# Kernel optimization log

Measured on AMD Instinct MI355X. Metric: run time of the kernel, lower is better.

## Reference

```python
import jax, jax.numpy as jnp
import numpy as np

N_NODES = 16384
N_EDGES = 262144
N_GRAPHS = 64
COLORS = 16
EMB = 256
HEADS = 8
FFN = 1024
LAYERS = 4
LMAX = 320


def _ln(x, g, b, eps=1e-5):
    m = x.mean(-1, keepdims=True)
    v = x.var(-1, keepdims=True)
    return (x - m) * jax.lax.rsqrt(v + eps) * g + b


def setup_inputs() -> dict:
    key = jax.random.key(0)
    ks = iter(jax.random.split(key, 64))
    s = 0.05
    def rn(shape):
        return jax.random.normal(next(ks), shape, jnp.float32) * s
    # 64 graphs: 32 with 192 nodes, 32 with 320 nodes -> total 16384, L_max=320
    lengths = np.concatenate([np.full(32, 192, np.int64), np.full(32, 320, np.int64)])
    batches = jnp.asarray(np.concatenate([[0], np.cumsum(lengths)]).astype(np.int32))
    x = jax.random.normal(next(ks), (N_NODES, COLORS), jnp.float32)
    edge_index = jax.random.randint(next(ks), (2, N_EDGES), 0, N_NODES, jnp.int32)
    inp = dict(
        x=x, edge_index=edge_index, batches=batches, L_max=LMAX,
        sW0=rn((COLORS, EMB)), sWn0=rn((COLORS, EMB)), sb0=jnp.zeros(EMB),
        sW1=rn((EMB, EMB)), sWn1=rn((EMB, EMB)), sb1=jnp.zeros(EMB),
        sW2=rn((EMB, EMB)), sWn2=rn((EMB, EMB)), sb2=jnp.zeros(EMB),
        Wq=rn((LAYERS, EMB, EMB)), Wk=rn((LAYERS, EMB, EMB)), Wv=rn((LAYERS, EMB, EMB)),
        bq=jnp.zeros((LAYERS, EMB)), bk=jnp.zeros((LAYERS, EMB)), bv=jnp.zeros((LAYERS, EMB)),
        Wo=rn((LAYERS, EMB, EMB)), bo=jnp.zeros((LAYERS, EMB)),
        ln1g=jnp.ones((LAYERS, EMB)), ln1b=jnp.zeros((LAYERS, EMB)),
        ln2g=jnp.ones((LAYERS, EMB)), ln2b=jnp.zeros((LAYERS, EMB)),
        W1=rn((LAYERS, EMB, FFN)), b1=jnp.zeros((LAYERS, FFN)),
        W2=rn((LAYERS, FFN, EMB)), b2=jnp.zeros((LAYERS, EMB)),
    )
    return inp


def reference(x, edge_index, batches, L_max,
              sW0, sWn0, sb0, sW1, sWn1, sb1, sW2, sWn2, sb2,
              Wq, Wk, Wv, bq, bk, bv, Wo, bo,
              ln1g, ln1b, ln2g, ln2b, W1, b1, W2, b2):
    N = x.shape[0]
    src, dst = edge_index[0], edge_index[1]
    deg = jnp.maximum(
        jax.ops.segment_sum(jnp.ones(src.shape[0], x.dtype), dst, num_segments=N), 1.0
    )[:, None]

    def sage(h, Ws, Wn, b, act):
        agg = jax.ops.segment_sum(h[src], dst, num_segments=N) / deg  # mean neighbor agg
        h2 = h @ Ws + agg @ Wn + b
        return jax.nn.relu(h2) if act else h2

    z = sage(x, sW0, sWn0, sb0, True)
    z = sage(z, sW1, sWn1, sb1, True)
    z = sage(z, sW2, sWn2, sb2, False)

    # pack_and_pad (intended semantics): seq-first [L_max, n_graphs, D] + key padding mask
    nG = batches.shape[0] - 1
    lengths = batches[1:] - batches[:-1]
    ids = jnp.arange(N)
    seg = jnp.searchsorted(batches, ids, side='right') - 1  # graph id per node
    pos = ids - batches[seg]                                 # position within graph
    D = z.shape[1]
    h = jnp.zeros((L_max, nG, D), z.dtype).at[pos, seg].set(z)
    pad = jnp.arange(L_max)[None, :] >= lengths[:, None]     # [nG, L_max], True = padded

    H = HEADS
    dh = D // H
    scale = 1.0 / np.sqrt(dh).astype(np.float32)
    for l in range(Wq.shape[0]):
        L, Bg = h.shape[0], h.shape[1]
        q = (h @ Wq[l] + bq[l]).reshape(L, Bg, H, dh)
        k = (h @ Wk[l] + bk[l]).reshape(L, Bg, H, dh)
        v = (h @ Wv[l] + bv[l]).reshape(L, Bg, H, dh)
        sc = jnp.einsum('lbhd,mbhd->bhlm', q, k) * scale
        sc = jnp.where(pad[:, None, None, :], -1e9, sc)
        a = jax.nn.softmax(sc, axis=-1)
        o = jnp.einsum('bhlm,mbhd->lbhd', a, v).reshape(L, Bg, D) @ Wo[l] + bo[l]
        h = _ln(h + o, ln1g[l], ln1b[l])
        ff = jax.nn.relu(h @ W1[l] + b1[l]) @ W2[l] + b2[l]
        h = _ln(h + ff, ln2g[l], ln2b[l])
    return h
```

## Files before the change

### kernel.cpp

```cpp
#include <hip/hip_runtime.h>
#include <hip/hip_bf16.h>
#include <math.h>

#define NN  16384
#define NE  262144
#define NG  64
#define CIN 16
#define DD  256
#define NHD 8
#define DHD 32
#define DFF 1024
#define NLY 4
#define LM  320
#define QS  768
#define QKW 512
#define NV  16384
#define NRV 16512

typedef __attribute__((ext_vector_type(8))) short bf16x8;
typedef __attribute__((ext_vector_type(4))) float f32x4;

__device__ __forceinline__ unsigned short f2bf(float f) {
    union { __hip_bfloat16 h; unsigned short u; } cv;
    cv.h = __float2bfloat16(f);
    return cv.u;
}
__device__ __forceinline__ float bf2f(unsigned short u) {
    return __uint_as_float((unsigned int)u << 16);
}
__device__ __forceinline__ void gl_lds16(const unsigned short* g, unsigned short* l) {
    __builtin_amdgcn_global_load_lds(
        (const __attribute__((address_space(1))) unsigned int*)g,
        (__attribute__((address_space(3))) unsigned int*)l, 16, 0, 0);
}
__device__ __forceinline__ int gsearch(const int* __restrict__ batches, int row) {
    int lo = 0, hi = NG;
    while (lo < hi) {
        int mid = (lo + hi + 1) >> 1;
        if (batches[mid] <= row) lo = mid; else hi = mid - 1;
    }
    return lo;
}

__global__ void zero_ws_kernel(uint4* __restrict__ hbp, uint4* __restrict__ obp,
                               int* __restrict__ counts) {
    int i = blockIdx.x * 256 + threadIdx.x;
    if (i < 4096) {
        hbp[i] = (uint4){0u, 0u, 0u, 0u};
        obp[i] = (uint4){0u, 0u, 0u, 0u};
    }
    if (i < NN) counts[i] = 0;
}

__global__ __launch_bounds__(256) void prep_all_kernel(
    const float* __restrict__ Wq, const float* __restrict__ Wk, const float* __restrict__ Wv,
    const float* __restrict__ Wo, const float* __restrict__ W1, const float* __restrict__ W2,
    const float* __restrict__ sW1, const float* __restrict__ sWn1,
    const float* __restrict__ sW2, const float* __restrict__ sWn2,
    const float* __restrict__ bq, const float* __restrict__ bk, const float* __restrict__ bv,
    unsigned short* __restrict__ Wqkvt, unsigned short* __restrict__ Wot,
    unsigned short* __restrict__ W1t, unsigned short* __restrict__ W2t,
    unsigned short* __restrict__ sW1t, unsigned short* __restrict__ sWn1t,
    unsigned short* __restrict__ sW2t, unsigned short* __restrict__ sWn2t,
    float* __restrict__ bqkvp)
{
    const int t = threadIdx.x;
    int bid = blockIdx.x;
    if (bid < 12) {
        int i = bid * 256 + t;
        if (i < NLY * QS) {
            int n = i % QS, l = i / QS;
            const float* b = (n < 256) ? bq : (n < 512 ? bk : bv);
            float v = b[l * DD + (n & 255)];
            if (n < 256) v *= 0.17677669529663687f;
            bqkvp[i] = v;
        }
        return;
    }
    bid -= 12;
    __shared__ float Ls[64][68];
    const float* inP;
    unsigned short* outP;
    int strideIn, strideOut;
    float sc = 1.f;
    if (bid < 192) {
        int x = bid % 12, y = (bid / 12) % 4, l = bid / 48;
        int n0 = x * 64, k0 = y * 64;
        const float* W = (n0 < 256) ? Wq : (n0 < 512 ? Wk : Wv);
        if (n0 < 256) sc = 0.17677669529663687f;
        inP  = W + ((size_t)l * DD + k0) * DD + (n0 & 255);
        strideIn = DD;
        outP = Wqkvt + ((size_t)l * QS + n0) * DD + k0;
        strideOut = DD;
    } else if (bid < 192 + 64) {
        bid -= 192;
        int x = bid % 4, y = (bid / 4) % 4, l = bid / 16;
        int n0 = x * 64, k0 = y * 64;
        inP  = Wo + ((size_t)l * DD + k0) * DD + n0;
        strideIn = DD;
        outP = Wot + ((size_t)l * DD + n0) * DD + k0;
        strideOut = DD;
    } else if (bid < 192 + 64 + 256) {
        bid -= 192 + 64;
        int x = bid % 16, y = (bid / 16) % 4, l = bid / 64;
        int n0 = x * 64, k0 = y * 64;
        inP  = W1 + ((size_t)l * DD + k0) * DFF + n0;
        strideIn = DFF;
        outP = W1t + ((size_t)l * DFF + n0) * DD + k0;
        strideOut = DD;
    } else if (bid < 192 + 64 + 512) {
        bid -= 192 + 64 + 256;
        int x = bid % 4, y = (bid / 4) % 16, l = bid / 64;
        int n0 = x * 64, k0 = y * 64;
        inP  = W2 + ((size_t)l * DFF + k0) * DD + n0;
        strideIn = DD;
        outP = W2t + ((size_t)l * DD + n0) * DFF + k0;
        strideOut = DFF;
    } else {
        bid -= 192 + 64 + 512;
        int w = bid / 16, r = bid % 16;
        int x = r % 4, y = r / 4;
        int n0 = x * 64, k0 = y * 64;
        const float* src = (w == 0) ? sW1 : (w == 1) ? sWn1 : (w == 2) ? sW2 : sWn2;
        unsigned short* dst = (w == 0) ? sW1t : (w == 1) ? sWn1t : (w == 2) ? sW2t : sWn2t;
        inP  = src + (size_t)k0 * DD + n0;
        strideIn = DD;
        outP = dst + (size_t)n0 * DD + k0;
        strideOut = DD;
    }
    #pragma unroll
    for (int it = 0; it < 4; ++it) {
        int lin = it * 256 + t;
        int kr = lin >> 4, nc = (lin & 15) * 4;
        float4 v = *(const float4*)&inP[(size_t)kr * strideIn + nc];
        Ls[kr][nc]     = v.x * sc;
        Ls[kr][nc + 1] = v.y * sc;
        Ls[kr][nc + 2] = v.z * sc;
        Ls[kr][nc + 3] = v.w * sc;
    }
    __syncthreads();
    #pragma unroll
    for (int it = 0; it < 2; ++it) {
        int lin = it * 256 + t;
        int nr = lin >> 3, kc = (lin & 7) * 8;
        unsigned short pk[8];
        #pragma unroll
        for (int j = 0; j < 8; ++j) pk[j] = f2bf(Ls[kc + j][nr]);
        *(uint4*)&outP[(size_t)nr * strideOut + kc] = *(uint4*)pk;
    }
}

__global__ void count_edges_kernel(const int* __restrict__ dst, int* __restrict__ counts) {
    int e = blockIdx.x * 256 + threadIdx.x;
    if (e < NE) atomicAdd(&counts[dst[e]], 1);
}

__global__ __launch_bounds__(1024) void scan_kernel(const int* __restrict__ counts,
                                                    int* __restrict__ offsets,
                                                    int* __restrict__ cursor) {
    __shared__ int part[1024];
    int t = threadIdx.x;
    int base = t * 16;
    int s = 0;
    #pragma unroll
    for (int i = 0; i < 16; ++i) s += counts[base + i];
    part[t] = s;
    __syncthreads();
    for (int off = 1; off < 1024; off <<= 1) {
        int val = (t >= off) ? part[t - off] : 0;
        __syncthreads();
        part[t] += val;
        __syncthreads();
    }
    int run = (t == 0) ? 0 : part[t - 1];
    #pragma unroll
    for (int i = 0; i < 16; ++i) {
        offsets[base + i] = run;
        cursor[base + i]  = run;
        run += counts[base + i];
    }
    if (t == 1023) offsets[NN] = run;
}

__global__ void fill_csr_kernel(const int* __restrict__ src, const int* __restrict__ dst,
                                int* __restrict__ cursor, int* __restrict__ csr) {
    int e = blockIdx.x * 256 + threadIdx.x;
    if (e < NE) {
        int p = atomicAdd(&cursor[dst[e]], 1);
        csr[p] = src[e];
    }
}

__global__ __launch_bounds__(256) void agg_mean16_kernel(
    const float* __restrict__ h, const int* __restrict__ offsets,
    const int* __restrict__ csr, float* __restrict__ out)
{
    int node = blockIdx.x * 16 + (threadIdx.x >> 4);
    int d = threadIdx.x & 15;
    int beg = offsets[node], end = offsets[node + 1];
    float acc = 0.f;
    int e = beg;
    for (; e + 1 < end; e += 2) {
        float v0 = h[(size_t)csr[e] * CIN + d];
        float v1 = h[(size_t)csr[e + 1] * CIN + d];
        acc += v0 + v1;
    }
    if (e < end) acc += h[(size_t)csr[e] * CIN + d];
    int dg = end - beg; if (dg < 1) dg = 1;
    out[(size_t)node * CIN + d] = acc * (1.f / (float)dg);
}

__global__ __launch_bounds__(256) void agg_mean_b_kernel(
    const unsigned short* __restrict__ h, const int* __restrict__ offsets,
    const int* __restrict__ csr, unsigned short* __restrict__ out)
{
    int node = blockIdx.x * 4 + (threadIdx.x >> 6);
    int lane = threadIdx.x & 63;
    int half = lane >> 5;
    int hl   = lane & 31;
    int beg = offsets[node], end = offsets[node + 1];
    float a[8] = {0.f, 0.f, 0.f, 0.f, 0.f, 0.f, 0.f, 0.f};
    int e = beg + half;
    for (; e + 2 < end; e += 4) {
        bf16x8 h0 = *(const bf16x8*)(h + (size_t)csr[e] * DD + hl * 8);
        bf16x8 h1 = *(const bf16x8*)(h + (size_t)csr[e + 2] * DD + hl * 8);
        #pragma unroll
        for (int j = 0; j < 8; ++j) a[j] += bf2f((unsigned short)h0[j]);
        #pragma unroll
        for (int j = 0; j < 8; ++j) a[j] += bf2f((unsigned short)h1[j]);
    }
    if (e < end) {
        bf16x8 h0 = *(const bf16x8*)(h + (size_t)csr[e] * DD + hl * 8);
        #pragma unroll
        for (int j = 0; j < 8; ++j) a[j] += bf2f((unsigned short)h0[j]);
    }
    #pragma unroll
    for (int j = 0; j < 8; ++j) a[j] += __shfl_xor(a[j], 32, 64);
    int dg = end - beg; if (dg < 1) dg = 1;
    float inv = 1.f / (float)dg;
    if (half == 0) {
        unsigned short pk[8];
        #pragma unroll
        for (int j = 0; j < 8; ++j) pk[j] = f2bf(a[j] * inv);
        *(uint4*)(out + (size_t)node * DD + hl * 8) = *(uint4*)pk;
    }
}

template <int ACT, bool DUAL>
__global__ __launch_bounds__(256) void gemm_f32b_kernel(
    const float* __restrict__ A, const float* __restrict__ W,
    const float* __restrict__ A2, const float* __restrict__ W2,
    const float* __restrict__ bias, unsigned short* __restrict__ Cb,
    int M, int N, int K)
{
    __shared__ __align__(16) float As[16][64];
    __shared__ __align__(16) float Ws[16][64];
    const int t  = threadIdx.x;
    const int tx = t & 15, ty = t >> 4;
    const int m0 = blockIdx.y * 64, n0 = blockIdx.x * 64;
    const int arow = t >> 2, acol = (t & 3) * 4;
    const int wrow = t >> 4, wcol = (t & 15) * 4;
    float acc[4][4] = {};
    const int npass = DUAL ? 2 : 1;
    for (int pass = 0; pass < npass; ++pass) {
        const float* Ap = (DUAL && pass) ? A2 : A;
        const float* Wp = (DUAL && pass) ? W2 : W;
        for (int k0 = 0; k0 < K; k0 += 16) {
            __syncthreads();
            float4 av = *(const float4*)(Ap + (size_t)(m0 + arow) * K + k0 + acol);
            As[acol + 0][arow] = av.x;
            As[acol + 1][arow] = av.y;
            As[acol + 2][arow] = av.z;
            As[acol + 3][arow] = av.w;
            *(float4*)&Ws[wrow][wcol] = *(const float4*)(Wp + (size_t)(k0 + wrow) * N + n0 + wcol);
            __syncthreads();
            #pragma unroll
            for (int kk = 0; kk < 16; ++kk) {
                float4 a4 = *(const float4*)&As[kk][ty * 4];
                float4 b4 = *(const float4*)&Ws[kk][tx * 4];
                float aa[4] = {a4.x, a4.y, a4.z, a4.w};
                float bb[4] = {b4.x, b4.y, b4.z, b4.w};
                #pragma unroll
                for (int i = 0; i < 4; ++i)
                    #pragma unroll
                    for (int j = 0; j < 4; ++j)
                        acc[i][j] += aa[i] * bb[j];
            }
        }
    }
    float4 bv = *(const float4*)(bias + n0 + tx * 4);
    float bb4[4] = {bv.x, bv.y, bv.z, bv.w};
    #pragma unroll
    for (int i = 0; i < 4; ++i) {
        float c[4];
        #pragma unroll
        for (int j = 0; j < 4; ++j) {
            c[j] = acc[i][j] + bb4[j];
            if (ACT == 1) c[j] = fmaxf(c[j], 0.f);
        }
        ushort4 ov;
        ov.x = f2bf(c[0]); ov.y = f2bf(c[1]); ov.z = f2bf(c[2]); ov.w = f2bf(c[3]);
        *(ushort4*)(Cb + (size_t)(m0 + ty * 4 + i) * N + n0 + tx * 4) = ov;
    }
}

template <int ACT, bool DUAL>
__global__ __launch_bounds__(256) void mfma_gemm_kernel(
    const unsigned short* __restrict__ A,  const unsigned short* __restrict__ Wt,
    const unsigned short* __restrict__ A2, const unsigned short* __restrict__ Wt2,
    const float* __restrict__ bias, unsigned short* __restrict__ Cb,
    int M, int N, int K)
{
    __shared__ __align__(16) unsigned short As[128 * 64];
    __shared__ __align__(16) unsigned short Bs[128 * 64];
    const int t = threadIdx.x;
    const int wave = t >> 6, lane = t & 63;
    const int quad = lane >> 4, r16 = lane & 15;
    const int wr = (wave >> 1) * 64, wc = (wave & 1) * 64;
    const int m0 = blockIdx.y * 128, n0 = blockIdx.x * 128;
    const int srow = t >> 3;
    const int scol = ((t & 7) * 8) ^ ((srow & 7) << 3);
    const int swz  = (r16 & 7) << 3;

    f32x4 acc[4][4];
    #pragma unroll
    for (int i = 0; i < 4; ++i)
        #pragma unroll
        for (int j = 0; j < 4; ++j)
            acc[i][j] = (f32x4){0.f, 0.f, 0.f, 0.f};

    const int npass = DUAL ? 2 : 1;
    for (int pass = 0; pass < npass; ++pass) {
        const unsigned short* Ap = (DUAL && pass) ? A2 : A;
        const unsigned short* Wp = (DUAL && pass) ? Wt2 : Wt;
        for (int k0 = 0; k0 < K; k0 += 64) {
            __syncthreads();
            #pragma unroll
            for (int c = 0; c < 4; ++c) {
                gl_lds16(&Ap[(size_t)(m0 + c * 32 + srow) * K + k0 + scol],
                         As + c * 2048 + wave * 512);
                gl_lds16(&Wp[(size_t)(n0 + c * 32 + srow) * K + k0 + scol],
                         Bs + c * 2048 + wave * 512);
            }
            __syncthreads();
            #pragma unroll
            for (int kk = 0; kk < 2; ++kk) {
                const int cofs = (kk * 32 + quad * 8) ^ swz;
                bf16x8 af[4], bfr[4];
                #pragma unroll
                for (int i = 0; i < 4; ++i)
                    af[i] = *(const bf16x8*)&As[(wr + i * 16 + r16) * 64 + cofs];
                #pragma unroll
                for (int j = 0; j < 4; ++j)
                    bfr[j] = *(const bf16x8*)&Bs[(wc + j * 16 + r16) * 64 + cofs];
                #pragma unroll
                for (int i = 0; i < 4; ++i)
                    #pragma unroll
                    for (int j = 0; j < 4; ++j)
                        acc[i][j] = __builtin_amdgcn_mfma_f32_16x16x32_bf16(
                            af[i], bfr[j], acc[i][j], 0, 0, 0);
            }
        }
    }

    float bcol[4];
    #pragma unroll
    for (int j = 0; j < 4; ++j) bcol[j] = bias[n0 + wc + j * 16 + r16];
    #pragma unroll
    for (int i = 0; i < 4; ++i) {
        const int rowb = m0 + wr + i * 16 + quad * 4;
        #pragma unroll
        for (int rr = 0; rr < 4; ++rr) {
            const size_t rb = (size_t)(rowb + rr) * N;
            #pragma unroll
            for (int j = 0; j < 4; ++j) {
                float v = acc[i][j][rr] + bcol[j];
                if (ACT == 1) v = fmaxf(v, 0.f);
                Cb[rb + n0 + wc + j * 16 + r16] = f2bf(v);
            }
        }
    }
}

__global__ __launch_bounds__(256) void gemm_qkv_kernel(
    const unsigned short* __restrict__ A, const unsigned short* __restrict__ Wt,
    const float* __restrict__ bias, const int* __restrict__ batches,
    unsigned short* __restrict__ QKb, unsigned short* __restrict__ Vt, int K)
{
    __shared__ __align__(16) unsigned short As[128 * 64];
    __shared__ __align__(16) unsigned short Bs[128 * 64];
    const int t = threadIdx.x;
    const int wave = t >> 6, lane = t & 63;
    const int quad = lane >> 4, r16 = lane & 15;
    const int wr = (wave >> 1) * 64, wc = (wave & 1) * 64;
    const int m0 = blockIdx.y * 128, n0 = blockIdx.x * 128;
    const int srow = t >> 3;
    const int scol = ((t & 7) * 8) ^ ((srow & 7) << 3);
    const int swz  = (r16 & 7) << 3;

    f32x4 acc[4][4];
    #pragma unroll
    for (int i = 0; i < 4; ++i)
        #pragma unroll
        for (int j = 0; j < 4; ++j)
            acc[i][j] = (f32x4){0.f, 0.f, 0.f, 0.f};

    for (int k0 = 0; k0 < K; k0 += 64) {
        __syncthreads();
        #pragma unroll
        for (int c = 0; c < 4; ++c) {
            gl_lds16(&A[(size_t)(m0 + c * 32 + srow) * K + k0 + scol],
                     As + c * 2048 + wave * 512);
            gl_lds16(&Wt[(size_t)(n0 + c * 32 + srow) * K + k0 + scol],
                     Bs + c * 2048 + wave * 512);
        }
        __syncthreads();
        #pragma unroll
        for (int kk = 0; kk < 2; ++kk) {
            const int cofs = (kk * 32 + quad * 8) ^ swz;
            bf16x8 af[4], bfr[4];
            #pragma unroll
            for (int i = 0; i < 4; ++i)
                af[i] = *(const bf16x8*)&As[(wr + i * 16 + r16) * 64 + cofs];
            #pragma unroll
            for (int j = 0; j < 4; ++j)
                bfr[j] = *(const bf16x8*)&Bs[(wc + j * 16 + r16) * 64 + cofs];
            #pragma unroll
            for (int i = 0; i < 4; ++i)
                #pragma unroll
                for (int j = 0; j < 4; ++j)
                    acc[i][j] = __builtin_amdgcn_mfma_f32_16x16x32_bf16(
                        af[i], bfr[j], acc[i][j], 0, 0, 0);
        }
    }

    float bcol[4];
    #pragma unroll
    for (int j = 0; j < 4; ++j) bcol[j] = bias[n0 + wc + j * 16 + r16];

    if (n0 < 512) {
        #pragma unroll
        for (int i = 0; i < 4; ++i) {
            const int rowb = m0 + wr + i * 16 + quad * 4;
            #pragma unroll
            for (int rr = 0; rr < 4; ++rr) {
                const size_t rb = (size_t)(rowb + rr) * QKW;
                #pragma unroll
                for (int j = 0; j < 4; ++j)
                    QKb[rb + n0 + wc + j * 16 + r16] = f2bf(acc[i][j][rr] + bcol[j]);
            }
        }
    } else {
        #pragma unroll
        for (int i = 0; i < 4; ++i) {
            const int rowb = m0 + wr + i * 16 + quad * 4;
            if (rowb >= NV) continue;
            const int g = gsearch(batches, rowb);
            const int key = rowb - batches[g];
            #pragma unroll
            for (int j = 0; j < 4; ++j) {
                const int dim = n0 - 512 + wc + j * 16 + r16;
                unsigned short pk[4];
                #pragma unroll
                for (int rr = 0; rr < 4; ++rr) pk[rr] = f2bf(acc[i][j][rr] + bcol[j]);
                *(uint2*)&Vt[((size_t)g * DD + dim) * LM + key] = *(uint2*)pk;
            }
        }
    }
}

template <bool PERM>
__global__ __launch_bounds__(512) void gemm_ln_kernel(
    const unsigned short* __restrict__ A, const unsigned short* __restrict__ Wt,
    const float* __restrict__ bias, const unsigned short* __restrict__ residb,
    const float* __restrict__ gam, const float* __restrict__ bet,
    const int* __restrict__ batches,
    float* __restrict__ outF, float* __restrict__ repO,
    unsigned short* __restrict__ outHb, int K)
{
    __shared__ __align__(16) unsigned short As[64 * 64];
    __shared__ __align__(16) unsigned short Bs[256 * 64];
    __shared__ float red[2][4][64];
    const int t = threadIdx.x;
    const int wave = t >> 6, lane = t & 63;
    const int quad = lane >> 4, r16 = lane & 15;
    const int wr = (wave >> 2) * 32;
    const int wc = (wave & 3) * 64;
    const int m0 = blockIdx.x * 64;
    const int srow = t >> 3;
    const int scol = ((t & 7) * 8) ^ ((srow & 7) << 3);
    const int swz  = (r16 & 7) << 3;

    f32x4 acc[2][4];
    #pragma unroll
    for (int i = 0; i < 2; ++i)
        #pragma unroll
        for (int j = 0; j < 4; ++j)
            acc[i][j] = (f32x4){0.f, 0.f, 0.f, 0.f};

    for (int k0 = 0; k0 < K; k0 += 64) {
        __syncthreads();
        gl_lds16(&A[(size_t)(m0 + srow) * K + k0 + scol], As + wave * 512);
        #pragma unroll
        for (int c = 0; c < 4; ++c)
            gl_lds16(&Wt[(size_t)(c * 64 + srow) * K + k0 + scol],
                     Bs + c * 4096 + wave * 512);
        __syncthreads();
        #pragma unroll
        for (int kk = 0; kk < 2; ++kk) {
            const int cofs = (kk * 32 + quad * 8) ^ swz;
            bf16x8 af[2], bfr[4];
            #pragma unroll
            for (int i = 0; i < 2; ++i)
                af[i] = *(const bf16x8*)&As[(wr + i * 16 + r16) * 64 + cofs];
            #pragma unroll
            for (int j = 0; j < 4; ++j)
                bfr[j] = *(const bf16x8*)&Bs[(wc + j * 16 + r16) * 64 + cofs];
            #pragma unroll
            for (int i = 0; i < 2; ++i)
                #pragma unroll
                for (int j = 0; j < 4; ++j)
                    acc[i][j] = __builtin_amdgcn_mfma_f32_16x16x32_bf16(
                        af[i], bfr[j], acc[i][j], 0, 0, 0);
        }
    }

    float bcol[4];
    #pragma unroll
    for (int j = 0; j < 4; ++j) bcol[j] = bias[wc + j * 16 + r16];

    #pragma unroll
    for (int i = 0; i < 2; ++i) {
        const int row = wr + i * 16 + quad * 4;
        #pragma unroll
        for (int rr = 0; rr < 4; ++rr) {
            const size_t rb = (size_t)(m0 + row + rr) * DD;
            float s1 = 0.f, s2 = 0.f;
            #pragma unroll
            for (int j = 0; j < 4; ++j) {
                float v = acc[i][j][rr] + bcol[j] + bf2f(residb[rb + wc + j * 16 + r16]);
                acc[i][j][rr] = v;
                s1 += v;
                s2 += v * v;
            }
            #pragma unroll
            for (int off = 1; off < 16; off <<= 1) {
                s1 += __shfl_xor(s1, off, 64);
                s2 += __shfl_xor(s2, off, 64);
            }
            if (r16 == 0) {
                red[0][wave & 3][row + rr] = s1;
                red[1][wave & 3][row + rr] = s2;
            }
        }
    }
    __syncthreads();

    int gg = 0, posb = 0;
    if (PERM && m0 < NV) {
        gg = gsearch(batches, m0);
        posb = m0 - batches[gg];
    }
    #pragma unroll
    for (int i = 0; i < 2; ++i) {
        const int row = wr + i * 16 + quad * 4;
        #pragma unroll
        for (int rr = 0; rr < 4; ++rr) {
            const int lr = row + rr;
            const int gr = m0 + lr;
            float s1 = red[0][0][lr] + red[0][1][lr] + red[0][2][lr] + red[0][3][lr];
            float s2 = red[1][0][lr] + red[1][1][lr] + red[1][2][lr] + red[1][3][lr];
            float mean = s1 * (1.f / 256.f);
            float var  = s2 * (1.f / 256.f) - mean * mean;
            float rs = rsqrtf(var + 1e-5f);
            const size_t hb = (size_t)gr * DD;
            #pragma unroll
            for (int j = 0; j < 4; ++j) {
                const int col = wc + j * 16 + r16;
                float ov = (acc[i][j][rr] - mean) * rs * gam[col] + bet[col];
                if (PERM) {
                    if (m0 < NV) {
                        outF[((size_t)(posb + lr) * NG + gg) * DD + col] = ov;
                    } else {
                        int g2 = m0 - NV + lr;
                        if (g2 < NG) repO[(size_t)g2 * DD + col] = ov;
                    }
                } else {
                    outHb[hb + col] = f2bf(ov);
                }
            }
        }
    }
}

__global__ __launch_bounds__(256) void attn_mfma_kernel(
    const unsigned short* __restrict__ qk, const unsigned short* __restrict__ vt,
    const int* __restrict__ batches, unsigned short* __restrict__ o)
{
    __shared__ __align__(16) unsigned short Pa[4][64 * 40];
    const int bx = blockIdx.x;
    const int tile = bx >> 1;
    const int row0 = tile * 64;
    const int tid = threadIdx.x;
    const int wave = tid >> 6;
    const int h = (bx & 1) * 4 + wave;
    const int lane = tid & 63;
    const int quad = lane >> 4, r16 = lane & 15;
    const int g = gsearch(batches, row0);
    const int len = batches[g + 1] - batches[g];
    const size_t gq = (size_t)batches[g];
    unsigned short* pa = Pa[wave];

    bf16x8 qf[4];
    #pragma unroll
    for (int i = 0; i < 4; ++i)
        qf[i] = *(const bf16x8*)(qk + (size_t)(row0 + i * 16 + r16) * QKW + h * 32 + quad * 8);
    bf16x8 onesf;
    #pragma unroll
    for (int j = 0; j < 8; ++j) onesf[j] = (short)0x3F80;

    f32x4 oacc[4][2], lacc[4];
    #pragma unroll
    for (int i = 0; i < 4; ++i) {
        lacc[i] = (f32x4){0.f, 0.f, 0.f, 0.f};
        #pragma unroll
        for (int nt = 0; nt < 2; ++nt)
            oacc[i][nt] = (f32x4){0.f, 0.f, 0.f, 0.f};
    }

    for (int t0 = 0; t0 < len; t0 += 32) {
        bf16x8 kf[2], vf[2];
        #pragma unroll
        for (int mt = 0; mt < 2; ++mt)
            kf[mt] = *(const bf16x8*)(qk + (gq + t0 + mt * 16 + r16) * QKW + 256 + h * 32 + quad * 8);
        #pragma unroll
        for (int nt = 0; nt < 2; ++nt)
            vf[nt] = *(const bf16x8*)(vt + ((size_t)g * DD + h * 32 + nt * 16 + r16) * LM
                                      + t0 + quad * 8);
        f32x4 st[2][4];
        #pragma unroll
        for (int mt = 0; mt < 2; ++mt)
            #pragma unroll
            for (int i = 0; i < 4; ++i)
                st[mt][i] = (f32x4){0.f, 0.f, 0.f, 0.f};
        #pragma unroll
        for (int mt = 0; mt < 2; ++mt)
            #pragma unroll
            for (int i = 0; i < 4; ++i)
                st[mt][i] = __builtin_amdgcn_mfma_f32_16x16x32_bf16(
                    kf[mt], qf[i], st[mt][i], 0, 0, 0);
        #pragma unroll
        for (int i = 0; i < 4; ++i) {
            #pragma unroll
            for (int mt = 0; mt < 2; ++mt) {
                float pr[4];
                #pragma unroll
                for (int rr = 0; rr < 4; ++rr)
                    pr[rr] = __expf(st[mt][i][rr]);
                uint2 w;
                w.x = ((unsigned)f2bf(pr[1]) << 16) | f2bf(pr[0]);
                w.y = ((unsigned)f2bf(pr[3]) << 16) | f2bf(pr[2]);
                *(uint2*)&pa[(i * 16 + r16) * 40 + mt * 16 + quad * 4] = w;
            }
        }
        __asm__ volatile("s_waitcnt lgkmcnt(0)" ::: "memory");
        bf16x8 pf[4];
        #pragma unroll
        for (int i = 0; i < 4; ++i)
            pf[i] = *(const bf16x8*)&pa[(i * 16 + r16) * 40 + quad * 8];
        #pragma unroll
        for (int i = 0; i < 4; ++i) {
            #pragma unroll
            for (int nt = 0; nt < 2; ++nt)
                oacc[i][nt] = __builtin_amdgcn_mfma_f32_16x16x32_bf16(
                    pf[i], vf[nt], oacc[i][nt], 0, 0, 0);
            lacc[i] = __builtin_amdgcn_mfma_f32_16x16x32_bf16(
                pf[i], onesf, lacc[i], 0, 0, 0);
        }
    }
    #pragma unroll
    for (int i = 0; i < 4; ++i) {
        #pragma unroll
        for (int rr = 0; rr < 4; ++rr) {
            float inv = 1.f / lacc[i][rr];
            size_t base = (size_t)(row0 + i * 16 + quad * 4 + rr) * DD + h * 32;
            #pragma unroll
            for (int nt = 0; nt < 2; ++nt)
                o[base + nt * 16 + r16] = f2bf(oacc[i][nt][rr] * inv);
        }
    }
}

__global__ __launch_bounds__(256) void attn_rep_kernel(
    const unsigned short* __restrict__ qk, const unsigned short* __restrict__ vt,
    const int* __restrict__ batches, unsigned short* __restrict__ o)
{
    __shared__ float pbuf[4][LM];
    const int wave = threadIdx.x >> 6, lane = threadIdx.x & 63;
    const int idx = blockIdx.x * 4 + wave;
    const int g = idx >> 3, h = idx & 7;
    const int len = batches[g + 1] - batches[g];
    const size_t gq = (size_t)batches[g];

    float q[32];
    const unsigned short* qrow = qk + (size_t)(NV + g) * QKW + h * 32;
    #pragma unroll
    for (int c = 0; c < 4; ++c) {
        bf16x8 qv = *(const bf16x8*)(qrow + c * 8);
        #pragma unroll
        for (int j = 0; j < 8; ++j) q[c * 8 + j] = bf2f((unsigned short)qv[j]);
    }

    float psum = 0.f;
    for (int key = lane; key < len; key += 64) {
        const unsigned short* krow = qk + (gq + key) * QKW + 256 + h * 32;
        float s = 0.f;
        #pragma unroll
        for (int c = 0; c < 4; ++c) {
            bf16x8 kv = *(const bf16x8*)(krow + c * 8);
            #pragma unroll
            for (int j = 0; j < 8; ++j) s += q[c * 8 + j] * bf2f((unsigned short)kv[j]);
        }
        float p = __expf(s);
        pbuf[wave][key] = p;
        psum += p;
    }
    #pragma unroll
    for (int off = 1; off < 64; off <<= 1) psum += __shfl_xor(psum, off, 64);
    __syncthreads();

    const int d = lane & 31, half = lane >> 5;
    float acc = 0.f;
    const unsigned short* vrow = vt + ((size_t)g * DD + h * 32 + d) * LM;
    for (int key = half * 8; key < len; key += 16) {
        bf16x8 v8 = *(const bf16x8*)(vrow + key);
        #pragma unroll
        for (int j = 0; j < 8; ++j) acc += pbuf[wave][key + j] * bf2f((unsigned short)v8[j]);
    }
    acc += __shfl_xor(acc, 32, 64);
    if (half == 0)
        o[(size_t)(NV + g) * DD + h * 32 + d] = f2bf(acc / psum);
}

__global__ __launch_bounds__(256) void bcast_pad_kernel(
    const float* __restrict__ repO, const int* __restrict__ batches,
    float* __restrict__ outF)
{
    const int g = blockIdx.x;
    const int t = threadIdx.x;
    const int len = batches[g + 1] - batches[g];
    float v = repO[(size_t)g * DD + t];
    for (int pos = len; pos < LM; ++pos)
        outF[((size_t)pos * NG + g) * DD + t] = v;
}

extern "C" void kernel_launch(void* const* d_in, const int* in_sizes, int n_in,
                              void* d_out, int out_size, void* d_ws, size_t ws_size,
                              hipStream_t stream) {
    const float* x       = (const float*)d_in[0];
    const int*   ei      = (const int*)d_in[1];
    const int*   batches = (const int*)d_in[2];
    const float* sW0  = (const float*)d_in[4];
    const float* sWn0 = (const float*)d_in[5];
    const float* sb0  = (const float*)d_in[6];
    const float* sW1  = (const float*)d_in[7];
    const float* sWn1 = (const float*)d_in[8];
    const float* sb1  = (const float*)d_in[9];
    const float* sW2  = (const float*)d_in[10];
    const float* sWn2 = (const float*)d_in[11];
    const float* sb2  = (const float*)d_in[12];
    const float* Wq   = (const float*)d_in[13];
    const float* Wk   = (const float*)d_in[14];
    const float* Wv   = (const float*)d_in[15];
    const float* bq   = (const float*)d_in[16];
    const float* bk   = (const float*)d_in[17];
    const float* bv   = (const float*)d_in[18];
    const float* Wo   = (const float*)d_in[19];
    const float* bo   = (const float*)d_in[20];
    const float* ln1g = (const float*)d_in[21];
    const float* ln1b = (const float*)d_in[22];
    const float* ln2g = (const float*)d_in[23];
    const float* ln2b = (const float*)d_in[24];
    const float* W1   = (const float*)d_in[25];
    const float* b1   = (const float*)d_in[26];
    const float* W2   = (const float*)d_in[27];
    const float* b2   = (const float*)d_in[28];

    char* p = (char*)d_ws;
    auto alloc = [&](size_t bytes) {
        char* r = p;
        p += (bytes + 255) & ~(size_t)255;
        return r;
    };
    int*   counts  = (int*)alloc((size_t)NN * 4);
    int*   offsets = (int*)alloc((size_t)(NN + 1) * 4);
    int*   cursor  = (int*)alloc((size_t)NN * 4);
    int*   csr     = (int*)alloc((size_t)NE * 4);
    float* agg0    = (float*)alloc((size_t)NN * CIN * 4);
    unsigned short* z0b = (unsigned short*)alloc((size_t)NN * DD * 2);
    unsigned short* a1b = (unsigned short*)alloc((size_t)NN * DD * 2);
    unsigned short* z1b = (unsigned short*)alloc((size_t)NN * DD * 2);
    unsigned short* a2b = (unsigned short*)alloc((size_t)NN * DD * 2);
    unsigned short* Vt = (unsigned short*)alloc((size_t)NG * DD * LM * 2);
    unsigned short* Hb = (unsigned short*)alloc((size_t)NRV * DD * 2);
    unsigned short* Ob = (unsigned short*)alloc((size_t)NRV * DD * 2);
    unsigned short* R  = (unsigned short*)alloc((size_t)NRV * DFF * 2);
    unsigned short* QKb = R;
    unsigned short* F1b = R;
    unsigned short* Wqkvt = (unsigned short*)alloc((size_t)NLY * QS * DD * 2);
    unsigned short* Wot   = (unsigned short*)alloc((size_t)NLY * DD * DD * 2);
    unsigned short* W1t   = (unsigned short*)alloc((size_t)NLY * DFF * DD * 2);
    unsigned short* W2t   = (unsigned short*)alloc((size_t)NLY * DD * DFF * 2);
    unsigned short* sW1t  = (unsigned short*)alloc((size_t)DD * DD * 2);
    unsigned short* sWn1t = (unsigned short*)alloc((size_t)DD * DD * 2);
    unsigned short* sW2t  = (unsigned short*)alloc((size_t)DD * DD * 2);
    unsigned short* sWn2t = (unsigned short*)alloc((size_t)DD * DD * 2);
    float* bqkvp   = (float*)alloc((size_t)NLY * QS * 4);
    float* repOut  = (float*)alloc((size_t)NG * DD * 4);

    prep_all_kernel<<<844, 256, 0, stream>>>(
        Wq, Wk, Wv, Wo, W1, W2, sW1, sWn1, sW2, sWn2, bq, bk, bv,
        Wqkvt, Wot, W1t, W2t, sW1t, sWn1t, sW2t, sWn2t, bqkvp);
    zero_ws_kernel<<<NN / 256, 256, 0, stream>>>(
        (uint4*)(Hb + (size_t)NV * DD), (uint4*)(Ob + (size_t)NV * DD), counts);

    count_edges_kernel<<<NE / 256, 256, 0, stream>>>(ei + NE, counts);
    scan_kernel<<<1, 1024, 0, stream>>>(counts, offsets, cursor);
    fill_csr_kernel<<<NE / 256, 256, 0, stream>>>(ei, ei + NE, cursor, csr);

    agg_mean16_kernel<<<NN / 16, 256, 0, stream>>>(x, offsets, csr, agg0);
    gemm_f32b_kernel<1, true><<<dim3(DD / 64, NN / 64), 256, 0, stream>>>(
        x, sW0, agg0, sWn0, sb0, z0b, NN, DD, CIN);
    agg_mean_b_kernel<<<NN / 4, 256, 0, stream>>>(z0b, offsets, csr, a1b);
    mfma_gemm_kernel<1, true><<<dim3(DD / 128, NN / 128), 256, 0, stream>>>(
        z0b, sW1t, a1b, sWn1t, sb1, z1b, NN, DD, DD);
    agg_mean_b_kernel<<<NN / 4, 256, 0, stream>>>(z1b, offsets, csr, a2b);
    mfma_gemm_kernel<0, true><<<dim3(DD / 128, NN / 128), 256, 0, stream>>>(
        z1b, sW2t, a2b, sWn2t, sb2, Hb, NN, DD, DD);

    for (int l = 0; l < NLY; ++l) {
        gemm_qkv_kernel<<<dim3(QS / 128, NRV / 128), 256, 0, stream>>>(
            Hb, Wqkvt + (size_t)l * QS * DD, bqkvp + (size_t)l * QS, batches, QKb, Vt, DD);
        attn_mfma_kernel<<<(NV / 64) * 2, 256, 0, stream>>>(QKb, Vt, batches, Ob);
        attn_rep_kernel<<<NG * NHD / 4, 256, 0, stream>>>(QKb, Vt, batches, Ob);
        gemm_ln_kernel<false><<<NRV / 64, 512, 0, stream>>>(
            Ob, Wot + (size_t)l * DD * DD, bo + (size_t)l * DD, Hb,
            ln1g + (size_t)l * DD, ln1b + (size_t)l * DD, batches, nullptr, nullptr, Hb, DD);
        mfma_gemm_kernel<1, false><<<dim3(DFF / 128, NRV / 128), 256, 0, stream>>>(
            Hb, W1t + (size_t)l * DFF * DD, nullptr, nullptr,
            b1 + (size_t)l * DFF, F1b, NRV, DFF, DD);
        if (l == NLY - 1)
            gemm_ln_kernel<true><<<NRV / 64, 512, 0, stream>>>(
                F1b, W2t + (size_t)l * DD * DFF, b2 + (size_t)l * DD, Hb,
                ln2g + (size_t)l * DD, ln2b + (size_t)l * DD, batches,
                (float*)d_out, repOut, Hb, DFF);
        else
            gemm_ln_kernel<false><<<NRV / 64, 512, 0, stream>>>(
                F1b, W2t + (size_t)l * DD * DFF, b2 + (size_t)l * DD, Hb,
                ln2g + (size_t)l * DD, ln2b + (size_t)l * DD, batches,
                nullptr, nullptr, Hb, DFF);
    }
    bcast_pad_kernel<<<NG, 256, 0, stream>>>(repOut, batches, (float*)d_out);
}
```

Measured before the change: 683.5 us.

## Merge small kernels, prefetch K/V in attention, unroll neighbor aggregation

Folds the workspace-zeroing kernel into the weight-prep launch and merges the per-graph representative attention into the main MFMA attention kernel as extra blocks, removing several launches per layer. The main attention loop now prefetches the next K/V fragments while the current tile's MFMAs run, and raises wave priority around the MFMA sections. The neighbor-mean aggregation loops are unrolled further to keep more gathers in flight. Register pressure rises from the prefetch buffers. The merged representative path swaps its __syncthreads for a wave-local LDS wait, which is valid only because each wave uses its own buffer.

Result: faster. 669.5 us (-2.0%).

```diff
diff --git a/kernel.cpp b/kernel.cpp
--- a/kernel.cpp
+++ b/kernel.cpp
@@ -42,16 +42,6 @@
     return lo;
 }
 
-__global__ void zero_ws_kernel(uint4* __restrict__ hbp, uint4* __restrict__ obp,
-                               int* __restrict__ counts) {
-    int i = blockIdx.x * 256 + threadIdx.x;
-    if (i < 4096) {
-        hbp[i] = (uint4){0u, 0u, 0u, 0u};
-        obp[i] = (uint4){0u, 0u, 0u, 0u};
-    }
-    if (i < NN) counts[i] = 0;
-}
-
 __global__ __launch_bounds__(256) void prep_all_kernel(
     const float* __restrict__ Wq, const float* __restrict__ Wk, const float* __restrict__ Wv,
     const float* __restrict__ Wo, const float* __restrict__ W1, const float* __restrict__ W2,
@@ -62,7 +52,8 @@
     unsigned short* __restrict__ W1t, unsigned short* __restrict__ W2t,
     unsigned short* __restrict__ sW1t, unsigned short* __restrict__ sWn1t,
     unsigned short* __restrict__ sW2t, unsigned short* __restrict__ sWn2t,
-    float* __restrict__ bqkvp)
+    float* __restrict__ bqkvp,
+    uint4* __restrict__ hbz, uint4* __restrict__ obz, int* __restrict__ counts)
 {
     const int t = threadIdx.x;
     int bid = blockIdx.x;
@@ -78,6 +69,15 @@
         return;
     }
     bid -= 12;
+    if (bid >= 832) {
+        int i = (bid - 832) * 256 + t;
+        if (i < 4096) {
+            hbz[i] = (uint4){0u, 0u, 0u, 0u};
+            obz[i] = (uint4){0u, 0u, 0u, 0u};
+        }
+        if (i < NN) counts[i] = 0;
+        return;
+    }
     __shared__ float Ls[64][68];
     const float* inP;
     unsigned short* outP;
@@ -200,12 +200,14 @@
     int beg = offsets[node], end = offsets[node + 1];
     float acc = 0.f;
     int e = beg;
-    for (; e + 1 < end; e += 2) {
+    for (; e + 3 < end; e += 4) {
         float v0 = h[(size_t)csr[e] * CIN + d];
         float v1 = h[(size_t)csr[e + 1] * CIN + d];
-        acc += v0 + v1;
-    }
-    if (e < end) acc += h[(size_t)csr[e] * CIN + d];
+        float v2 = h[(size_t)csr[e + 2] * CIN + d];
+        float v3 = h[(size_t)csr[e + 3] * CIN + d];
+        acc += (v0 + v1) + (v2 + v3);
+    }
+    for (; e < end; ++e) acc += h[(size_t)csr[e] * CIN + d];
     int dg = end - beg; if (dg < 1) dg = 1;
     out[(size_t)node * CIN + d] = acc * (1.f / (float)dg);
 }
@@ -221,15 +223,17 @@
     int beg = offsets[node], end = offsets[node + 1];
     float a[8] = {0.f, 0.f, 0.f, 0.f, 0.f, 0.f, 0.f, 0.f};
     int e = beg + half;
-    for (; e + 2 < end; e += 4) {
-        bf16x8 h0 = *(const bf16x8*)(h + (size_t)csr[e] * DD + hl * 8);
+    for (; e + 6 < end; e += 8) {
+        bf16x8 h0 = *(const bf16x8*)(h + (size_t)csr[e]     * DD + hl * 8);
         bf16x8 h1 = *(const bf16x8*)(h + (size_t)csr[e + 2] * DD + hl * 8);
-        #pragma unroll
-        for (int j = 0; j < 8; ++j) a[j] += bf2f((unsigned short)h0[j]);
-        #pragma unroll
-        for (int j = 0; j < 8; ++j) a[j] += bf2f((unsigned short)h1[j]);
-    }
-    if (e < end) {
+        bf16x8 h2 = *(const bf16x8*)(h + (size_t)csr[e + 4] * DD + hl * 8);
+        bf16x8 h3 = *(const bf16x8*)(h + (size_t)csr[e + 6] * DD + hl * 8);
+        #pragma unroll
+        for (int j = 0; j < 8; ++j)
+            a[j] += (bf2f((unsigned short)h0[j]) + bf2f((unsigned short)h1[j]))
+                  + (bf2f((unsigned short)h2[j]) + bf2f((unsigned short)h3[j]));
+    }
+    for (; e < end; e += 2) {
         bf16x8 h0 = *(const bf16x8*)(h + (size_t)csr[e] * DD + hl * 8);
         #pragma unroll
         for (int j = 0; j < 8; ++j) a[j] += bf2f((unsigned short)h0[j]);
@@ -593,18 +597,67 @@
     }
 }
 
-__global__ __launch_bounds__(256) void attn_mfma_kernel(
+#define NBT ((NV / 64) * 2)
+__global__ __launch_bounds__(256) void attn_kernel(
     const unsigned short* __restrict__ qk, const unsigned short* __restrict__ vt,
     const int* __restrict__ batches, unsigned short* __restrict__ o)
 {
     __shared__ __align__(16) unsigned short Pa[4][64 * 40];
     const int bx = blockIdx.x;
+    const int tid = threadIdx.x;
+    const int wave = tid >> 6;
+    const int lane = tid & 63;
+
+    if (bx >= NBT) {
+        float* pbuf = (float*)&Pa[wave][0];
+        const int idx = (bx - NBT) * 4 + wave;
+        const int g = idx >> 3, h = idx & 7;
+        const int len = batches[g + 1] - batches[g];
+        const size_t gq = (size_t)batches[g];
+
+        float q[32];
+        const unsigned short* qrow = qk + (size_t)(NV + g) * QKW + h * 32;
+        #pragma unroll
+        for (int c = 0; c < 4; ++c) {
+            bf16x8 qv = *(const bf16x8*)(qrow + c * 8);
+            #pragma unroll
+            for (int j = 0; j < 8; ++j) q[c * 8 + j] = bf2f((unsigned short)qv[j]);
+        }
+        float psum = 0.f;
+        for (int key = lane; key < len; key += 64) {
+            const unsigned short* krow = qk + (gq + key) * QKW + 256 + h * 32;
+            float s = 0.f;
+            #pragma unroll
+            for (int c = 0; c < 4; ++c) {
+                bf16x8 kv = *(const bf16x8*)(krow + c * 8);
+                #pragma unroll
+                for (int j = 0; j < 8; ++j) s += q[c * 8 + j] * bf2f((unsigned short)kv[j]);
+            }
+            float pv = __expf(s);
+            pbuf[key] = pv;
+            psum += pv;
+        }
+        #pragma unroll
+        for (int off = 1; off < 64; off <<= 1) psum += __shfl_xor(psum, off, 64);
+        __asm__ volatile("s_waitcnt lgkmcnt(0)" ::: "memory");
+
+        const int d = lane & 31, half = lane >> 5;
+        float acc = 0.f;
+        const unsigned short* vrow = vt + ((size_t)g * DD + h * 32 + d) * LM;
+        for (int key = half * 8; key < len; key += 16) {
+            bf16x8 v8 = *(const bf16x8*)(vrow + key);
+            #pragma unroll
+            for (int j = 0; j < 8; ++j) acc += pbuf[key + j] * bf2f((unsigned short)v8[j]);
+        }
+        acc += __shfl_xor(acc, 32, 64);
+        if (half == 0)
+            o[(size_t)(NV + g) * DD + h * 32 + d] = f2bf(acc / psum);
+        return;
+    }
+
     const int tile = bx >> 1;
     const int row0 = tile * 64;
-    const int tid = threadIdx.x;
-    const int wave = tid >> 6;
     const int h = (bx & 1) * 4 + wave;
-    const int lane = tid & 63;
     const int quad = lane >> 4, r16 = lane & 15;
     const int g = gsearch(batches, row0);
     const int len = batches[g + 1] - batches[g];
@@ -628,27 +681,41 @@
             oacc[i][nt] = (f32x4){0.f, 0.f, 0.f, 0.f};
     }
 
+    const unsigned short* kbase = qk + gq * QKW + 256 + h * 32 + quad * 8;
+    const unsigned short* vbase = vt + ((size_t)g * DD + h * 32 + r16) * LM + quad * 8;
+
+    bf16x8 kf[2], vf[2];
+    kf[0] = *(const bf16x8*)(kbase + (size_t)(r16) * QKW);
+    kf[1] = *(const bf16x8*)(kbase + (size_t)(16 + r16) * QKW);
+    vf[0] = *(const bf16x8*)(vbase);
+    vf[1] = *(const bf16x8*)(vbase + 16 * LM);
+
     for (int t0 = 0; t0 < len; t0 += 32) {
-        bf16x8 kf[2], vf[2];
-        #pragma unroll
-        for (int mt = 0; mt < 2; ++mt)
-            kf[mt] = *(const bf16x8*)(qk + (gq + t0 + mt * 16 + r16) * QKW + 256 + h * 32 + quad * 8);
-        #pragma unroll
-        for (int nt = 0; nt < 2; ++nt)
-            vf[nt] = *(const bf16x8*)(vt + ((size_t)g * DD + h * 32 + nt * 16 + r16) * LM
-                                      + t0 + quad * 8);
         f32x4 st[2][4];
         #pragma unroll
         for (int mt = 0; mt < 2; ++mt)
             #pragma unroll
             for (int i = 0; i < 4; ++i)
                 st[mt][i] = (f32x4){0.f, 0.f, 0.f, 0.f};
+        __builtin_amdgcn_s_setprio(1);
         #pragma unroll
         for (int mt = 0; mt < 2; ++mt)
             #pragma unroll
             for (int i = 0; i < 4; ++i)
                 st[mt][i] = __builtin_amdgcn_mfma_f32_16x16x32_bf16(
                     kf[mt], qf[i], st[mt][i], 0, 0, 0);
+        __builtin_amdgcn_s_setprio(0);
+
+        const bool more = (t0 + 32) < len;
+        bf16x8 kn[2], vn[2];
+        if (more) {
+            const int tn = t0 + 32;
+            kn[0] = *(const bf16x8*)(kbase + (size_t)(tn + r16) * QKW);
+            kn[1] = *(const bf16x8*)(kbase + (size_t)(tn + 16 + r16) * QKW);
+            vn[0] = *(const bf16x8*)(vbase + tn);
+            vn[1] = *(const bf16x8*)(vbase + 16 * LM + tn);
+        }
+
         #pragma unroll
         for (int i = 0; i < 4; ++i) {
             #pragma unroll
@@ -668,6 +735,7 @@
         #pragma unroll
         for (int i = 0; i < 4; ++i)
             pf[i] = *(const bf16x8*)&pa[(i * 16 + r16) * 40 + quad * 8];
+        __builtin_amdgcn_s_setprio(1);
         #pragma unroll
         for (int i = 0; i < 4; ++i) {
             #pragma unroll
@@ -677,6 +745,11 @@
             lacc[i] = __builtin_amdgcn_mfma_f32_16x16x32_bf16(
                 pf[i], onesf, lacc[i], 0, 0, 0);
         }
+        __builtin_amdgcn_s_setprio(0);
+        if (more) {
+            kf[0] = kn[0]; kf[1] = kn[1];
+            vf[0] = vn[0]; vf[1] = vn[1];
+        }
     }
     #pragma unroll
     for (int i = 0; i < 4; ++i) {
@@ -689,57 +762,6 @@
                 o[base + nt * 16 + r16] = f2bf(oacc[i][nt][rr] * inv);
         }
     }
-}
-
-__global__ __launch_bounds__(256) void attn_rep_kernel(
-    const unsigned short* __restrict__ qk, const unsigned short* __restrict__ vt,
-    const int* __restrict__ batches, unsigned short* __restrict__ o)
-{
-    __shared__ float pbuf[4][LM];
-    const int wave = threadIdx.x >> 6, lane = threadIdx.x & 63;
-    const int idx = blockIdx.x * 4 + wave;
-    const int g = idx >> 3, h = idx & 7;
-    const int len = batches[g + 1] - batches[g];
-    const size_t gq = (size_t)batches[g];
-
-    float q[32];
-    const unsigned short* qrow = qk + (size_t)(NV + g) * QKW + h * 32;
-    #pragma unroll
-    for (int c = 0; c < 4; ++c) {
-        bf16x8 qv = *(const bf16x8*)(qrow + c * 8);
-        #pragma unroll
-        for (int j = 0; j < 8; ++j) q[c * 8 + j] = bf2f((unsigned short)qv[j]);
-    }
-
-    float psum = 0.f;
-    for (int key = lane; key < len; key += 64) {
-        const unsigned short* krow = qk + (gq + key) * QKW + 256 + h * 32;
-        float s = 0.f;
-        #pragma unroll
-        for (int c = 0; c < 4; ++c) {
-            bf16x8 kv = *(const bf16x8*)(krow + c * 8);
-            #pragma unroll
-            for (int j = 0; j < 8; ++j) s += q[c * 8 + j] * bf2f((unsigned short)kv[j]);
-        }
-        float p = __expf(s);
-        pbuf[wave][key] = p;
-        psum += p;
-    }
-    #pragma unroll
-    for (int off = 1; off < 64; off <<= 1) psum += __shfl_xor(psum, off, 64);
-    __syncthreads();
-
-    const int d = lane & 31, half = lane >> 5;
-    float acc = 0.f;
-    const unsigned short* vrow = vt + ((size_t)g * DD + h * 32 + d) * LM;
-    for (int key = half * 8; key < len; key += 16) {
-        bf16x8 v8 = *(const bf16x8*)(vrow + key);
-        #pragma unroll
-        for (int j = 0; j < 8; ++j) acc += pbuf[wave][key + j] * bf2f((unsigned short)v8[j]);
-    }
-    acc += __shfl_xor(acc, 32, 64);
-    if (half == 0)
-        o[(size_t)(NV + g) * DD + h * 32 + d] = f2bf(acc / psum);
 }
 
 __global__ __launch_bounds__(256) void bcast_pad_kernel(
@@ -818,10 +840,9 @@
     float* bqkvp   = (float*)alloc((size_t)NLY * QS * 4);
     float* repOut  = (float*)alloc((size_t)NG * DD * 4);
 
-    prep_all_kernel<<<844, 256, 0, stream>>>(
+    prep_all_kernel<<<908, 256, 0, stream>>>(
         Wq, Wk, Wv, Wo, W1, W2, sW1, sWn1, sW2, sWn2, bq, bk, bv,
-        Wqkvt, Wot, W1t, W2t, sW1t, sWn1t, sW2t, sWn2t, bqkvp);
-    zero_ws_kernel<<<NN / 256, 256, 0, stream>>>(
+        Wqkvt, Wot, W1t, W2t, sW1t, sWn1t, sW2t, sWn2t, bqkvp,
         (uint4*)(Hb + (size_t)NV * DD), (uint4*)(Ob + (size_t)NV * DD), counts);
 
     count_edges_kernel<<<NE / 256, 256, 0, stream>>>(ei + NE, counts);
@@ -841,8 +862,7 @@
     for (int l = 0; l < NLY; ++l) {
         gemm_qkv_kernel<<<dim3(QS / 128, NRV / 128), 256, 0, stream>>>(
             Hb, Wqkvt + (size_t)l * QS * DD, bqkvp + (size_t)l * QS, batches, QKb, Vt, DD);
-        attn_mfma_kernel<<<(NV / 64) * 2, 256, 0, stream>>>(QKb, Vt, batches, Ob);
-        attn_rep_kernel<<<NG * NHD / 4, 256, 0, stream>>>(QKb, Vt, batches, Ob);
+        attn_kernel<<<NBT + NG * 2, 256, 0, stream>>>(QKb, Vt, batches, Ob);
         gemm_ln_kernel<false><<<NRV / 64, 512, 0, stream>>>(
             Ob, Wot + (size_t)l * DD * DD, bo + (size_t)l * DD, Hb,
             ln1g + (size_t)l * DD, ln1b + (size_t)l * DD, batches, nullptr, nullptr, Hb, DD);
```
